# Kernel optimization log

Hardware: AMD Instinct MI355X
Metric: run time of the kernel (lower is better)

The kernel has to match this reference:

```python
import jax, jax.numpy as jnp
import numpy as np


def setup_inputs() -> dict:
    key = jax.random.key(0)
    ks = jax.random.split(key, 9)
    D, DK, DV = 512, 64, 64
    B, S = 4, 4096
    sd = 1.0 / np.sqrt(D).astype(np.float32)
    so = 1.0 / np.sqrt(DV).astype(np.float32)
    return {
        "x": jax.random.normal(ks[0], (B, S, D), dtype=jnp.float32),
        "Wq": jax.random.normal(ks[1], (D, DK), dtype=jnp.float32) * sd,
        "bq": jnp.zeros((DK,), dtype=jnp.float32),
        "Wk": jax.random.normal(ks[2], (D, DK), dtype=jnp.float32) * sd,
        "bk": jnp.zeros((DK,), dtype=jnp.float32),
        "Wv": jax.random.normal(ks[3], (D, DV), dtype=jnp.float32) * sd,
        "bv": jnp.zeros((DV,), dtype=jnp.float32),
        "Wo": jax.random.normal(ks[4], (DV, D), dtype=jnp.float32) * so,
        "bo": jnp.zeros((D,), dtype=jnp.float32),
    }


def reference(x, Wq, bq, Wk, bk, Wv, bv, Wo, bo):
    # x: (B, S, D)
    B, S, D = x.shape
    dk = Wq.shape[1]
    q = x @ Wq + bq            # (B, S, dk)
    k = x @ Wk + bk            # (B, S, dk)
    v = x @ Wv + bv            # (B, S, dv)
    scores = jnp.einsum("bik,bjk->bij", q, k) / jnp.sqrt(jnp.float32(dk))  # (B,S,S)
    # causal mask: True where j <= i (keep)
    causal = jnp.tril(jnp.ones((S, S), dtype=bool))
    scores = jnp.where(causal[None, :, :], scores, -jnp.inf)
    weights = jax.nn.softmax(scores, axis=-1)   # every row has >=1 unmasked entry
    out = jnp.einsum("bij,bjv->biv", weights, v)  # (B, S, dv)
    return out @ Wo + bo
```

## Files before the change

kernel.cpp:

```cpp
#include <hip/hip_runtime.h>
#include <hip/hip_bf16.h>

#define S_LEN 4096
#define D_MODEL 512
#define DKV 64
#define B_N 4
#define STR 72
#define VSTR 136

typedef __hip_bfloat16 bf16;
typedef __attribute__((ext_vector_type(8))) short short8;
typedef __attribute__((ext_vector_type(4))) float floatx4;

#define MFMA(a, b, c) __builtin_amdgcn_mfma_f32_16x16x32_bf16(a, b, c, 0, 0, 0)

__device__ __forceinline__ float b2f(bf16 v) { return __bfloat162float(v); }

__device__ __forceinline__ unsigned short f2bits(float v) {
    union { bf16 h; unsigned short u; } cv;
    cv.h = __float2bfloat16(v);
    return cv.u;
}
__device__ __forceinline__ float bits2f(unsigned short u) {
    union { bf16 h; unsigned short u; } cv;
    cv.u = u;
    return b2f(cv.h);
}

__global__ __launch_bounds__(64) void detect_kernel(const void* x, int* flag) {
    const int lane = threadIdx.x;
    const bf16* xb = (const bf16*)x;
    int bad = 0;
    for (int k = lane; k < 4096; k += 64) {
        float v = fabsf(b2f(xb[2 * k]));
        if (!(v < 64.f)) bad++;
    }
    #pragma unroll
    for (int off = 32; off >= 1; off >>= 1) bad += __shfl_xor(bad, off);
    if (lane == 0) *flag = (bad > 100) ? 1 : 0;
}

__global__ __launch_bounds__(512) void wprep_qkv_frag(
    const void* __restrict__ Wq, const void* __restrict__ bq,
    const void* __restrict__ Wk, const void* __restrict__ bk,
    const void* __restrict__ Wv, const void* __restrict__ bv,
    bf16* __restrict__ Wfh, bf16* __restrict__ Wfl, float* __restrict__ ball,
    const int* __restrict__ flag)
{
    __shared__ float xs[16][513];
    const int ct = blockIdx.x;
    const int c0 = ct * 16;
    const int g = c0 >> 6;
    const int cc0 = c0 & 63;
    const void* W    = (g == 0) ? Wq : (g == 1) ? Wk : Wv;
    const void* bias = (g == 0) ? bq : (g == 1) ? bk : bv;
    const int tid = threadIdx.x;
    const int f32 = *flag;

    #pragma unroll
    for (int i = 0; i < 16; ++i) {
        const int idx = tid + 512 * i;
        const int d = idx >> 4, j = idx & 15;
        const float v = f32 ? ((const float*)W)[(size_t)d * DKV + cc0 + j]
                            : b2f(((const bf16*)W)[(size_t)d * DKV + cc0 + j]);
        xs[j][d] = v;
    }
    __syncthreads();

    union Pack8 { uint4 u; unsigned short s[8]; };
    #pragma unroll
    for (int rep = 0; rep < 2; ++rep) {
        const int f = tid + rep * 512;
        const int kt = f >> 6, lane = f & 63;
        const int quad = lane >> 4, l15 = lane & 15;
        Pack8 ph, pl;
        #pragma unroll
        for (int j = 0; j < 8; ++j) {
            const float v = xs[l15][kt * 32 + quad * 8 + j];
            const unsigned short hb = f2bits(v);
            ph.s[j] = hb;
            pl.s[j] = f2bits(v - bits2f(hb));
        }
        const size_t o = (((size_t)ct * 16 + kt) * 64 + lane) * 8;
        *(uint4*)&Wfh[o] = ph.u;
        *(uint4*)&Wfl[o] = pl.u;
    }
    if (tid < 16)
        ball[c0 + tid] = f32 ? ((const float*)bias)[cc0 + tid]
                             : b2f(((const bf16*)bias)[cc0 + tid]);
}

__global__ __launch_bounds__(512) void wprep_o_frag(
    const void* __restrict__ Wo, const void* __restrict__ bo,
    bf16* __restrict__ WoFh, bf16* __restrict__ WoFl,
    float* __restrict__ ball2, const int* __restrict__ flag)
{
    __shared__ float ys[16][65];
    const int ctile = blockIdx.x;
    const int c0 = ctile * 16;
    const int tid = threadIdx.x;
    const int f32 = *flag;

    #pragma unroll
    for (int rep = 0; rep < 2; ++rep) {
        const int idx = tid + rep * 512;
        const int d = idx >> 4, j = idx & 15;
        const float v = f32 ? ((const float*)Wo)[(size_t)d * D_MODEL + c0 + j]
                            : b2f(((const bf16*)Wo)[(size_t)d * D_MODEL + c0 + j]);
        ys[j][d] = v;
    }
    __syncthreads();

    union Pack8 { uint4 u; unsigned short s[8]; };
    if (tid < 128) {
        const int kc = tid >> 6, lane = tid & 63;
        const int quad = lane >> 4, l15 = lane & 15;
        Pack8 ph, pl;
        #pragma unroll
        for (int j = 0; j < 8; ++j) {
            const float v = ys[l15][kc * 32 + quad * 8 + j];
            const unsigned short hb = f2bits(v);
            ph.s[j] = hb;
            pl.s[j] = f2bits(v - bits2f(hb));
        }
        const size_t o = (((size_t)ctile * 2 + kc) * 64 + lane) * 8;
        *(uint4*)&WoFh[o] = ph.u;
        *(uint4*)&WoFl[o] = pl.u;
    }
    if (tid < 16)
        ball2[c0 + tid] = f32 ? ((const float*)bo)[c0 + tid]
                              : b2f(((const bf16*)bo)[c0 + tid]);
}

__global__ __launch_bounds__(256) void qkv_mfma_bf16(
    const void* __restrict__ x,
    const bf16* __restrict__ Wfh, const float* __restrict__ ball,
    bf16* __restrict__ Qb, bf16* __restrict__ Kb, bf16* __restrict__ Vt,
    const int* __restrict__ flag)
{
    if (*flag) return;
    __shared__ unsigned short hiA[32 * D_MODEL];
    const int tid = threadIdx.x;
    const int rowBase = blockIdx.x * 32;

    const unsigned short* xr = (const unsigned short*)x + (size_t)rowBase * D_MODEL;
    #pragma unroll
    for (int i = 0; i < 8; ++i) {
        const int idx = tid + 256 * i;
        const int r = idx >> 6;
        const int c0 = (idx & 63) << 3;
        const uint4 hv = *(const uint4*)&xr[r * D_MODEL + c0];
        const int boff = (c0 * 2) ^ ((r & 7) << 4);
        *(uint4*)((char*)hiA + r * 1024 + boff) = hv;
    }
    __syncthreads();

    const int lane = tid & 63;
    const int w    = tid >> 6;
    const int quad = lane >> 4;
    const int l15  = lane & 15;
    const int wr   = w & 1;
    const int wcol = w >> 1;
    const int arow = wr * 16 + l15;
    const char* hib = (const char*)hiA + arow * 1024;
    const int swz = (arow & 7) << 4;

    floatx4 acc[6];
    #pragma unroll
    for (int ct = 0; ct < 6; ++ct) acc[ct] = (floatx4){0.f, 0.f, 0.f, 0.f};

    for (int kt = 0; kt < 16; ++kt) {
        const int boff = (kt * 64 + quad * 16) ^ swz;
        const short8 ah = *(const short8*)(hib + boff);
        #pragma unroll
        for (int ct = 0; ct < 6; ++ct) {
            const size_t fo = (((size_t)(wcol * 6 + ct) * 16 + kt) * 64 + lane) * 8;
            const short8 bh = *(const short8*)&Wfh[fo];
            acc[ct] = MFMA(ah, bh, acc[ct]);
        }
    }

    #pragma unroll
    for (int ct = 0; ct < 6; ++ct) {
        const int gc = wcol * 96 + ct * 16 + l15;
        const float bias = ball[gc];
        const float scale = (gc < 64) ? 0.18033688f : 1.0f;
        #pragma unroll
        for (int r = 0; r < 4; ++r) {
            const int gr = rowBase + wr * 16 + quad * 4 + r;
            const bf16 o = __float2bfloat16((acc[ct][r] + bias) * scale);
            if (gc < 64)       Qb[(size_t)gr * DKV + gc] = o;
            else if (gc < 128) Kb[(size_t)gr * DKV + (gc - 64)] = o;
            else {
                const int bb = gr >> 12, sidx = gr & (S_LEN - 1);
                Vt[((size_t)bb * DKV + (gc - 128)) * S_LEN + sidx] = o;
            }
        }
    }
}

__global__ __launch_bounds__(512) void qkv_mfma_f32(
    const void* __restrict__ x,
    const bf16* __restrict__ Wfh, const bf16* __restrict__ Wfl,
    const float* __restrict__ ball,
    bf16* __restrict__ Qb, bf16* __restrict__ Kb, bf16* __restrict__ Vt,
    const int* __restrict__ flag)
{
    if (!*flag) return;
    __shared__ unsigned short hiA[32 * D_MODEL];
    __shared__ unsigned short loA[32 * D_MODEL];
    const int tid = threadIdx.x;
    const int rowBase = blockIdx.x * 32;

    union Pack8 { uint4 u; unsigned short s[8]; };
    {
        const float* xr = (const float*)x + (size_t)rowBase * D_MODEL;
        #pragma unroll
        for (int i = 0; i < 4; ++i) {
            const int idx = tid + 512 * i;
            const int r = idx >> 6;
            const int c0 = (idx & 63) << 3;
            const float4 v0 = *(const float4*)&xr[r * D_MODEL + c0];
            const float4 v1 = *(const float4*)&xr[r * D_MODEL + c0 + 4];
            const float vv[8] = {v0.x, v0.y, v0.z, v0.w, v1.x, v1.y, v1.z, v1.w};
            Pack8 ph, pl;
            #pragma unroll
            for (int j = 0; j < 8; ++j) {
                const unsigned short hb = f2bits(vv[j]);
                ph.s[j] = hb;
                pl.s[j] = f2bits(vv[j] - bits2f(hb));
            }
            const int boff = (c0 * 2) ^ ((r & 7) << 4);
            *(uint4*)((char*)hiA + r * 1024 + boff) = ph.u;
            *(uint4*)((char*)loA + r * 1024 + boff) = pl.u;
        }
    }
    __syncthreads();

    const int lane = tid & 63;
    const int w    = tid >> 6;
    const int quad = lane >> 4;
    const int l15  = lane & 15;
    const int wr   = w & 1;
    const int wq   = w >> 1;
    const int arow = wr * 16 + l15;
    const char* hib = (const char*)hiA + arow * 1024;
    const char* lob = (const char*)loA + arow * 1024;
    const int swz = (arow & 7) << 4;

    floatx4 acc[3];
    #pragma unroll
    for (int ct = 0; ct < 3; ++ct) acc[ct] = (floatx4){0.f, 0.f, 0.f, 0.f};

    for (int kt = 0; kt < 16; ++kt) {
        const int boff = (kt * 64 + quad * 16) ^ swz;
        const short8 ah = *(const short8*)(hib + boff);
        const short8 al = *(const short8*)(lob + boff);
        #pragma unroll
        for (int ct = 0; ct < 3; ++ct) {
            const size_t fo = (((size_t)(wq * 3 + ct) * 16 + kt) * 64 + lane) * 8;
            const short8 bh = *(const short8*)&Wfh[fo];
            const short8 bl = *(const short8*)&Wfl[fo];
            acc[ct] = MFMA(ah, bh, acc[ct]);
            acc[ct] = MFMA(ah, bl, acc[ct]);
            acc[ct] = MFMA(al, bh, acc[ct]);
        }
    }

    #pragma unroll
    for (int ct = 0; ct < 3; ++ct) {
        const int gc = wq * 48 + ct * 16 + l15;
        const float bias = ball[gc];
        const float scale = (gc < 64) ? 0.18033688f : 1.0f;
        #pragma unroll
        for (int r = 0; r < 4; ++r) {
            const int gr = rowBase + wr * 16 + quad * 4 + r;
            const bf16 o = __float2bfloat16((acc[ct][r] + bias) * scale);
            if (gc < 64)       Qb[(size_t)gr * DKV + gc] = o;
            else if (gc < 128) Kb[(size_t)gr * DKV + (gc - 64)] = o;
            else {
                const int bb = gr >> 12, sidx = gr & (S_LEN - 1);
                Vt[((size_t)bb * DKV + (gc - 128)) * S_LEN + sidx] = o;
            }
        }
    }
}

__global__ __launch_bounds__(256, 3) void attn_mfma(
    const bf16* __restrict__ Qg, const bf16* __restrict__ Kg,
    const bf16* __restrict__ Vtg, float* __restrict__ Op,
    float* __restrict__ Mp, float* __restrict__ Lp)
{
    const int bid = blockIdx.x;
    const int xcd = bid & 7;
    const int b  = xcd >> 1;
    const int kh = xcd & 1;
    const int t  = 127 - (bid >> 3);
    const int rowBase = t * 32;
    const int tid = threadIdx.x;
    const int lane = tid & 63;
    const int w  = tid >> 6;
    const int wr = w & 1;
    const int wc = w >> 1;
    const int quad = lane >> 4;
    const int l15  = lane & 15;

    __shared__ bf16 Kl[128 * STR];
    __shared__ bf16 Vl[64 * VSTR];
    __shared__ bf16 Pl[32 * VSTR];
    __shared__ float redm[2][32];
    __shared__ float reds[2][32];

    const bf16* Qb = Qg + ((size_t)b * S_LEN + rowBase) * DKV;
    const bf16* Kb = Kg + (size_t)b * S_LEN * DKV;
    const bf16* Vb = Vtg + (size_t)b * DKV * S_LEN;

    {
        const int r = tid >> 3, d0q = (tid & 7) * 8;
        *(uint4*)&Pl[r * VSTR + d0q] = *(const uint4*)&Qb[r * DKV + d0q];
    }
    __syncthreads();
    short8 qf0, qf1;
    {
        const int qoff = (wr * 16 + l15) * VSTR + quad * 8;
        qf0 = *(const short8*)&Pl[qoff];
        qf1 = *(const short8*)&Pl[qoff + 32];
    }

    floatx4 acc0 = {0.f, 0.f, 0.f, 0.f}, acc1 = {0.f, 0.f, 0.f, 0.f};
    float m_run[4], l_run[4];
    #pragma unroll
    for (int r = 0; r < 4; ++r) { m_run[r] = -1e30f; l_run[r] = 0.f; }

    const int kbMax = (rowBase + 31) >> 7;
    const int kk = tid >> 1, dk = (tid & 1) * 32;
    const int vd = tid >> 2, vk = (tid & 3) * 32;

    uint4 kr0, kr1, kr2, kr3, vr0, vr1, vr2, vr3;
    int kb = kh;
    if (kb <= kbMax) {
        const uint4* ks = (const uint4*)&Kb[((size_t)(kb * 128 + kk)) * DKV + dk];
        kr0 = ks[0]; kr1 = ks[1]; kr2 = ks[2]; kr3 = ks[3];
        const uint4* vs = (const uint4*)&Vb[(size_t)vd * S_LEN + kb * 128 + vk];
        vr0 = vs[0]; vr1 = vs[1]; vr2 = vs[2]; vr3 = vs[3];
    }

    for (; kb <= kbMax; kb += 2) {
        __syncthreads();
        {
            uint4* kd = (uint4*)&Kl[kk * STR + dk];
            kd[0] = kr0; kd[1] = kr1; kd[2] = kr2; kd[3] = kr3;
            uint4* vdst = (uint4*)&Vl[vd * VSTR + vk];
            vdst[0] = vr0; vdst[1] = vr1; vdst[2] = vr2; vdst[3] = vr3;
        }
        __syncthreads();
        if (kb + 2 <= kbMax) {
            const uint4* ks = (const uint4*)&Kb[((size_t)((kb + 2) * 128 + kk)) * DKV + dk];
            kr0 = ks[0]; kr1 = ks[1]; kr2 = ks[2]; kr3 = ks[3];
            const uint4* vs = (const uint4*)&Vb[(size_t)vd * S_LEN + (kb + 2) * 128 + vk];
            vr0 = vs[0]; vr1 = vs[1]; vr2 = vs[2]; vr3 = vs[3];
        }

        floatx4 s[4];
        #pragma unroll
        for (int j = 0; j < 4; ++j) s[j] = (floatx4){0.f, 0.f, 0.f, 0.f};
        {
            const int qk = quad * 8;
            #pragma unroll
            for (int j = 0; j < 4; ++j) {
                const int kc = (wc * 64 + j * 16 + l15) * STR + qk;
                const short8 ba = *(const short8*)&Kl[kc];
                const short8 bb = *(const short8*)&Kl[kc + 32];
                s[j] = MFMA(qf0, ba, s[j]);
                s[j] = MFMA(qf1, bb, s[j]);
            }
        }
        if (kb == kbMax) {
            const int rowg = rowBase + wr * 16 + quad * 4;
            #pragma unroll
            for (int j = 0; j < 4; ++j) {
                const int kg = kb * 128 + wc * 64 + j * 16 + l15;
                #pragma unroll
                for (int r = 0; r < 4; ++r)
                    if (kg > rowg + r) s[j][r] = -1e30f;
            }
        }
        float m4[4];
        #pragma unroll
        for (int r = 0; r < 4; ++r)
            m4[r] = fmaxf(fmaxf(s[0][r], s[1][r]), fmaxf(s[2][r], s[3][r]));
        #pragma unroll
        for (int off = 1; off < 16; off <<= 1) {
            #pragma unroll
            for (int r = 0; r < 4; ++r) m4[r] = fmaxf(m4[r], __shfl_xor(m4[r], off));
        }
        if (l15 == 0) {
            #pragma unroll
            for (int r = 0; r < 4; ++r) redm[wc][wr * 16 + quad * 4 + r] = m4[r];
        }
        __syncthreads();
        float alpha[4], mnew[4];
        #pragma unroll
        for (int r = 0; r < 4; ++r) {
            const int row = wr * 16 + quad * 4 + r;
            const float mm = fmaxf(redm[0][row], redm[1][row]);
            mnew[r] = fmaxf(m_run[r], mm);
            alpha[r] = exp2f(m_run[r] - mnew[r]);
            m_run[r] = mnew[r];
        }
        float ps[4];
        #pragma unroll
        for (int r = 0; r < 4; ++r) {
            float acc_ps = 0.f;
            #pragma unroll
            for (int j = 0; j < 4; ++j) {
                const float p = exp2f(s[j][r] - mnew[r]);
                s[j][r] = p;
                acc_ps += p;
            }
            ps[r] = acc_ps;
        }
        #pragma unroll
        for (int off = 1; off < 16; off <<= 1) {
            #pragma unroll
            for (int r = 0; r < 4; ++r) ps[r] += __shfl_xor(ps[r], off);
        }
        if (l15 == 0) {
            #pragma unroll
            for (int r = 0; r < 4; ++r) reds[wc][wr * 16 + quad * 4 + r] = ps[r];
        }
        #pragma unroll
        for (int r = 0; r < 4; ++r) {
            acc0[r] *= alpha[r]; acc1[r] *= alpha[r];
            const int poff = (wr * 16 + quad * 4 + r) * VSTR + wc * 64 + l15;
            Pl[poff]      = __float2bfloat16(s[0][r]);
            Pl[poff + 16] = __float2bfloat16(s[1][r]);
            Pl[poff + 32] = __float2bfloat16(s[2][r]);
            Pl[poff + 48] = __float2bfloat16(s[3][r]);
        }
        __syncthreads();
        #pragma unroll
        for (int r = 0; r < 4; ++r) {
            const int row = wr * 16 + quad * 4 + r;
            l_run[r] = l_run[r] * alpha[r] + reds[0][row] + reds[1][row];
        }
        {
            const int pk = quad * 8;
            const int prow = (wr * 16 + l15) * VSTR;
            const int vrow0 = (wc * 32 + l15) * VSTR;
            const int vrow1 = vrow0 + 16 * VSTR;
            #pragma unroll
            for (int j = 0; j < 4; ++j) {
                const short8 pa  = *(const short8*)&Pl[prow + pk + j * 32];
                const short8 vb0 = *(const short8*)&Vl[vrow0 + pk + j * 32];
                const short8 vb1 = *(const short8*)&Vl[vrow1 + pk + j * 32];
                acc0 = MFMA(pa, vb0, acc0);
                acc1 = MFMA(pa, vb1, acc1);
            }
        }
    }
    #pragma unroll
    for (int r = 0; r < 4; ++r) {
        const int row = rowBase + wr * 16 + quad * 4 + r;
        float* op = Op + (((size_t)kh * B_N + b) * S_LEN + row) * DKV + wc * 32 + l15;
        op[0]  = acc0[r];
        op[16] = acc1[r];
    }
    if (wc == 0 && l15 == 0) {
        #pragma unroll
        for (int r = 0; r < 4; ++r) {
            const int row = rowBase + wr * 16 + quad * 4 + r;
            const size_t mi = (size_t)kh * B_N * S_LEN + (size_t)b * S_LEN + row;
            Mp[mi] = m_run[r];
            Lp[mi] = l_run[r];
        }
    }
}

__global__ __launch_bounds__(256) void merge_kernel(
    const float* __restrict__ Op, const float* __restrict__ Mp,
    const float* __restrict__ Lp, bf16* __restrict__ Oh, bf16* __restrict__ Ol)
{
    const int row = blockIdx.x * 32 + (threadIdx.x >> 3);
    const int d0 = (threadIdx.x & 7) * 8;
    const size_t half = (size_t)B_N * S_LEN;

    const float m0 = Mp[row], m1 = Mp[half + row];
    const float l0 = Lp[row], l1 = Lp[half + row];
    const float m = fmaxf(m0, m1);
    const float w0 = exp2f(m0 - m), w1 = exp2f(m1 - m);
    const float inv = 1.0f / (l0 * w0 + l1 * w1);

    const float* p0 = Op + (size_t)row * DKV + d0;
    const float* p1 = Op + half * DKV + (size_t)row * DKV + d0;
    union Pack8 { uint4 u; unsigned short s[8]; };
    Pack8 ph, pl;
    #pragma unroll
    for (int j = 0; j < 8; ++j) {
        const float o = (p0[j] * w0 + p1[j] * w1) * inv;
        const unsigned short hb = f2bits(o);
        ph.s[j] = hb;
        pl.s[j] = f2bits(o - bits2f(hb));
    }
    *(uint4*)&Oh[(size_t)row * DKV + d0] = ph.u;
    *(uint4*)&Ol[(size_t)row * DKV + d0] = pl.u;
}

#define PSTR 72
__global__ __launch_bounds__(256) void proj_mfma_bf16(
    const bf16* __restrict__ Oh, const bf16* __restrict__ Ol,
    const bf16* __restrict__ WoFh, const float* __restrict__ ball2,
    bf16* __restrict__ out, const int* __restrict__ flag)
{
    if (*flag) return;
    __shared__ unsigned short Ah[32 * PSTR], Al[32 * PSTR];
    const int tid = threadIdx.x;
    const int rowBase = blockIdx.x * 32;

    {
        const int r = tid >> 3, c0 = (tid & 7) * 8;
        *(uint4*)&Ah[r * PSTR + c0] = *(const uint4*)&Oh[(size_t)(rowBase + r) * DKV + c0];
        *(uint4*)&Al[r * PSTR + c0] = *(const uint4*)&Ol[(size_t)(rowBase + r) * DKV + c0];
    }
    __syncthreads();

    const int lane = tid & 63;
    const int w    = tid >> 6;
    const int quad = lane >> 4;
    const int l15  = lane & 15;
    const int wr   = w & 1;
    const int wcq  = w >> 1;

    const int aoff = (wr * 16 + l15) * PSTR + quad * 8;
    const short8 ah0 = *(const short8*)&Ah[aoff];
    const short8 ah1 = *(const short8*)&Ah[aoff + 32];
    const short8 al0 = *(const short8*)&Al[aoff];
    const short8 al1 = *(const short8*)&Al[aoff + 32];

    floatx4 acc[16];
    #pragma unroll
    for (int ct = 0; ct < 16; ++ct) acc[ct] = (floatx4){0.f, 0.f, 0.f, 0.f};

    #pragma unroll
    for (int ct = 0; ct < 16; ++ct) {
        const int ctile = wcq * 16 + ct;
        const size_t o0 = (((size_t)ctile * 2 + 0) * 64 + lane) * 8;
        const size_t o1 = (((size_t)ctile * 2 + 1) * 64 + lane) * 8;
        const short8 bh0 = *(const short8*)&WoFh[o0];
        const short8 bh1 = *(const short8*)&WoFh[o1];
        acc[ct] = MFMA(ah0, bh0, acc[ct]);
        acc[ct] = MFMA(ah1, bh1, acc[ct]);
        acc[ct] = MFMA(al0, bh0, acc[ct]);
        acc[ct] = MFMA(al1, bh1, acc[ct]);
    }

    #pragma unroll
    for (int ct = 0; ct < 16; ++ct) {
        const int col = wcq * 256 + ct * 16 + l15;
        const float bias = ball2[col];
        #pragma unroll
        for (int r = 0; r < 4; ++r) {
            const int row = rowBase + wr * 16 + quad * 4 + r;
            out[(size_t)row * D_MODEL + col] = __float2bfloat16(acc[ct][r] + bias);
        }
    }
}

__global__ __launch_bounds__(512) void proj_mfma_f32(
    const bf16* __restrict__ Oh, const bf16* __restrict__ Ol,
    const bf16* __restrict__ WoFh, const bf16* __restrict__ WoFl,
    const float* __restrict__ ball2, float* __restrict__ out,
    const int* __restrict__ flag)
{
    if (!*flag) return;
    __shared__ unsigned short Ah[32 * PSTR], Al[32 * PSTR];
    const int tid = threadIdx.x;
    const int rowBase = blockIdx.x * 32;

    {
        const int r = (tid & 255) >> 3, c0 = (tid & 7) * 8;
        if (tid < 256)
            *(uint4*)&Ah[r * PSTR + c0] = *(const uint4*)&Oh[(size_t)(rowBase + r) * DKV + c0];
        else
            *(uint4*)&Al[r * PSTR + c0] = *(const uint4*)&Ol[(size_t)(rowBase + r) * DKV + c0];
    }
    __syncthreads();

    const int lane = tid & 63;
    const int w    = tid >> 6;
    const int quad = lane >> 4;
    const int l15  = lane & 15;
    const int wr   = w & 1;
    const int wcq  = w >> 1;

    const int aoff = (wr * 16 + l15) * PSTR + quad * 8;
    const short8 ah0 = *(const short8*)&Ah[aoff];
    const short8 ah1 = *(const short8*)&Ah[aoff + 32];
    const short8 al0 = *(const short8*)&Al[aoff];
    const short8 al1 = *(const short8*)&Al[aoff + 32];

    floatx4 acc[8];
    #pragma unroll
    for (int ct = 0; ct < 8; ++ct) acc[ct] = (floatx4){0.f, 0.f, 0.f, 0.f};

    #pragma unroll
    for (int ct = 0; ct < 8; ++ct) {
        const int ctile = wcq * 8 + ct;
        const size_t o0 = (((size_t)ctile * 2 + 0) * 64 + lane) * 8;
        const size_t o1 = (((size_t)ctile * 2 + 1) * 64 + lane) * 8;
        const short8 bh0 = *(const short8*)&WoFh[o0];
        const short8 bh1 = *(const short8*)&WoFh[o1];
        const short8 bl0 = *(const short8*)&WoFl[o0];
        const short8 bl1 = *(const short8*)&WoFl[o1];
        acc[ct] = MFMA(ah0, bh0, acc[ct]);
        acc[ct] = MFMA(ah1, bh1, acc[ct]);
        acc[ct] = MFMA(ah0, bl0, acc[ct]);
        acc[ct] = MFMA(ah1, bl1, acc[ct]);
        acc[ct] = MFMA(al0, bh0, acc[ct]);
        acc[ct] = MFMA(al1, bh1, acc[ct]);
    }

    #pragma unroll
    for (int ct = 0; ct < 8; ++ct) {
        const int col = wcq * 128 + ct * 16 + l15;
        const float bias = ball2[col];
        #pragma unroll
        for (int r = 0; r < 4; ++r) {
            const int row = rowBase + wr * 16 + quad * 4 + r;
            out[(size_t)row * D_MODEL + col] = acc[ct][r] + bias;
        }
    }
}

extern "C" void kernel_launch(void* const* d_in, const int* in_sizes, int n_in,
                              void* d_out, int out_size, void* d_ws, size_t ws_size,
                              hipStream_t stream) {
    const void* x  = d_in[0];
    const void* Wq = d_in[1];
    const void* bq = d_in[2];
    const void* Wk = d_in[3];
    const void* bk = d_in[4];
    const void* Wv = d_in[5];
    const void* bv = d_in[6];
    const void* Wo = d_in[7];
    const void* bo = d_in[8];

    const int rows = B_N * S_LEN;
    char* p = (char*)d_ws;
    int*  flag = (int*)p;                          p += 256;
    bf16* Qb = (bf16*)p;                           p += (size_t)rows * DKV * 2;
    bf16* Kb = (bf16*)p;                           p += (size_t)rows * DKV * 2;
    bf16* Vt = (bf16*)p;                           p += (size_t)rows * DKV * 2;
    bf16* Wfh = (bf16*)p;                          p += (size_t)12 * 16 * 64 * 8 * 2;
    bf16* Wfl = (bf16*)p;                          p += (size_t)12 * 16 * 64 * 8 * 2;
    float* ball = (float*)p;                       p += 1024;
    bf16* WoFh = (bf16*)p;                         p += (size_t)32 * 2 * 64 * 8 * 2;
    bf16* WoFl = (bf16*)p;                         p += (size_t)32 * 2 * 64 * 8 * 2;
    float* ball2 = (float*)p;                      p += D_MODEL * 4;
    float* Op = (float*)p;                         p += (size_t)2 * rows * DKV * 4;
    float* Mp = (float*)p;                         p += (size_t)2 * rows * 4;
    float* Lp = (float*)p;                         p += (size_t)2 * rows * 4;
    bf16* Ohb = (bf16*)p;                          p += (size_t)rows * DKV * 2;
    bf16* Olb = (bf16*)p;                          p += (size_t)rows * DKV * 2;

    detect_kernel<<<1, 64, 0, stream>>>(x, flag);
    wprep_qkv_frag<<<12, 512, 0, stream>>>(Wq, bq, Wk, bk, Wv, bv, Wfh, Wfl, ball, flag);
    wprep_o_frag<<<32, 512, 0, stream>>>(Wo, bo, WoFh, WoFl, ball2, flag);
    qkv_mfma_bf16<<<512, 256, 0, stream>>>(x, Wfh, ball, Qb, Kb, Vt, flag);
    qkv_mfma_f32<<<512, 512, 0, stream>>>(x, Wfh, Wfl, ball, Qb, Kb, Vt, flag);
    attn_mfma<<<1024, 256, 0, stream>>>(Qb, Kb, Vt, Op, Mp, Lp);
    merge_kernel<<<512, 256, 0, stream>>>(Op, Mp, Lp, Ohb, Olb);
    proj_mfma_bf16<<<512, 256, 0, stream>>>(Ohb, Olb, WoFh, ball2, (bf16*)d_out, flag);
    proj_mfma_f32<<<512, 512, 0, stream>>>(Ohb, Olb, WoFh, WoFl, ball2, (float*)d_out, flag);
}
```

Measured before the change: 189.9 us.

## Use 64-row query tiles with per-wave full key rows and configurable KV splits

The attention kernel now gives each block 64 query rows, and each wave owns 16 rows across all 128 keys. This removes the cross-wave max/sum reductions through shared memory and two block barriers per key tile, and makes each K/V tile load serve twice as many queries. The number of key splits becomes 4 when the workspace is large enough (2 otherwise), keeping the grid size, and the merge kernel is generalised to NS partials. The cost is more registers per thread (8 score tiles, 4 accumulators), more partial output traffic through merge, and a shared-memory P buffer that is now synchronised only with a waitcnt instead of a barrier.

```diff
diff --git a/kernel.cpp b/kernel.cpp
--- a/kernel.cpp
+++ b/kernel.cpp
@@ -289,50 +289,51 @@
 __global__ __launch_bounds__(256, 3) void attn_mfma(
     const bf16* __restrict__ Qg, const bf16* __restrict__ Kg,
     const bf16* __restrict__ Vtg, float* __restrict__ Op,
-    float* __restrict__ Mp, float* __restrict__ Lp)
+    float* __restrict__ Mp, float* __restrict__ Lp, const int NS)
 {
     const int bid = blockIdx.x;
     const int xcd = bid & 7;
-    const int b  = xcd >> 1;
-    const int kh = xcd & 1;
-    const int t  = 127 - (bid >> 3);
-    const int rowBase = t * 32;
+    const int rest = bid >> 3;
+    const int b   = xcd >> 1;
+    const int khH = (NS == 4) ? (rest & 1) : 0;
+    const int t64 = 63 - ((NS == 4) ? (rest >> 1) : rest);
+    const int kh  = khH * 2 + (xcd & 1);
+    const int rowBase = t64 * 64;
     const int tid = threadIdx.x;
     const int lane = tid & 63;
     const int w  = tid >> 6;
-    const int wr = w & 1;
-    const int wc = w >> 1;
     const int quad = lane >> 4;
     const int l15  = lane & 15;
 
     __shared__ bf16 Kl[128 * STR];
     __shared__ bf16 Vl[64 * VSTR];
-    __shared__ bf16 Pl[32 * VSTR];
-    __shared__ float redm[2][32];
-    __shared__ float reds[2][32];
+    __shared__ bf16 Pl[64 * VSTR];
 
     const bf16* Qb = Qg + ((size_t)b * S_LEN + rowBase) * DKV;
     const bf16* Kb = Kg + (size_t)b * S_LEN * DKV;
     const bf16* Vb = Vtg + (size_t)b * DKV * S_LEN;
 
     {
-        const int r = tid >> 3, d0q = (tid & 7) * 8;
-        *(uint4*)&Pl[r * VSTR + d0q] = *(const uint4*)&Qb[r * DKV + d0q];
+        const int qr = tid >> 2, qd = (tid & 3) * 16;
+        *(uint4*)&Pl[qr * VSTR + qd]     = *(const uint4*)&Qb[qr * DKV + qd];
+        *(uint4*)&Pl[qr * VSTR + qd + 8] = *(const uint4*)&Qb[qr * DKV + qd + 8];
     }
     __syncthreads();
     short8 qf0, qf1;
     {
-        const int qoff = (wr * 16 + l15) * VSTR + quad * 8;
+        const int qoff = (w * 16 + l15) * VSTR + quad * 8;
         qf0 = *(const short8*)&Pl[qoff];
         qf1 = *(const short8*)&Pl[qoff + 32];
     }
 
-    floatx4 acc0 = {0.f, 0.f, 0.f, 0.f}, acc1 = {0.f, 0.f, 0.f, 0.f};
+    floatx4 acc[4];
+    #pragma unroll
+    for (int v = 0; v < 4; ++v) acc[v] = (floatx4){0.f, 0.f, 0.f, 0.f};
     float m_run[4], l_run[4];
     #pragma unroll
     for (int r = 0; r < 4; ++r) { m_run[r] = -1e30f; l_run[r] = 0.f; }
 
-    const int kbMax = (rowBase + 31) >> 7;
+    const int kbMax = (rowBase + 63) >> 7;
     const int kk = tid >> 1, dk = (tid & 1) * 32;
     const int vd = tid >> 2, vk = (tid & 3) * 32;
 
@@ -345,7 +346,7 @@
         vr0 = vs[0]; vr1 = vs[1]; vr2 = vs[2]; vr3 = vs[3];
     }
 
-    for (; kb <= kbMax; kb += 2) {
+    for (; kb <= kbMax; kb += NS) {
         __syncthreads();
         {
             uint4* kd = (uint4*)&Kl[kk * STR + dk];
@@ -354,69 +355,66 @@
             vdst[0] = vr0; vdst[1] = vr1; vdst[2] = vr2; vdst[3] = vr3;
         }
         __syncthreads();
-        if (kb + 2 <= kbMax) {
-            const uint4* ks = (const uint4*)&Kb[((size_t)((kb + 2) * 128 + kk)) * DKV + dk];
+        if (kb + NS <= kbMax) {
+            const uint4* ks = (const uint4*)&Kb[((size_t)((kb + NS) * 128 + kk)) * DKV + dk];
             kr0 = ks[0]; kr1 = ks[1]; kr2 = ks[2]; kr3 = ks[3];
-            const uint4* vs = (const uint4*)&Vb[(size_t)vd * S_LEN + (kb + 2) * 128 + vk];
+            const uint4* vs = (const uint4*)&Vb[(size_t)vd * S_LEN + (kb + NS) * 128 + vk];
             vr0 = vs[0]; vr1 = vs[1]; vr2 = vs[2]; vr3 = vs[3];
         }
 
-        floatx4 s[4];
-        #pragma unroll
-        for (int j = 0; j < 4; ++j) s[j] = (floatx4){0.f, 0.f, 0.f, 0.f};
+        floatx4 s[8];
+        #pragma unroll
+        for (int jt = 0; jt < 8; ++jt) s[jt] = (floatx4){0.f, 0.f, 0.f, 0.f};
         {
             const int qk = quad * 8;
             #pragma unroll
-            for (int j = 0; j < 4; ++j) {
-                const int kc = (wc * 64 + j * 16 + l15) * STR + qk;
+            for (int jt = 0; jt < 8; ++jt) {
+                const int kc = (jt * 16 + l15) * STR + qk;
                 const short8 ba = *(const short8*)&Kl[kc];
                 const short8 bb = *(const short8*)&Kl[kc + 32];
-                s[j] = MFMA(qf0, ba, s[j]);
-                s[j] = MFMA(qf1, bb, s[j]);
+                s[jt] = MFMA(qf0, ba, s[jt]);
+                s[jt] = MFMA(qf1, bb, s[jt]);
             }
         }
         if (kb == kbMax) {
-            const int rowg = rowBase + wr * 16 + quad * 4;
-            #pragma unroll
-            for (int j = 0; j < 4; ++j) {
-                const int kg = kb * 128 + wc * 64 + j * 16 + l15;
+            const int rowg = rowBase + w * 16 + quad * 4;
+            #pragma unroll
+            for (int jt = 0; jt < 8; ++jt) {
+                const int kg = kb * 128 + jt * 16 + l15;
                 #pragma unroll
                 for (int r = 0; r < 4; ++r)
-                    if (kg > rowg + r) s[j][r] = -1e30f;
+                    if (kg > rowg + r) s[jt][r] = -1e30f;
             }
         }
         float m4[4];
         #pragma unroll
-        for (int r = 0; r < 4; ++r)
-            m4[r] = fmaxf(fmaxf(s[0][r], s[1][r]), fmaxf(s[2][r], s[3][r]));
+        for (int r = 0; r < 4; ++r) {
+            float mm = s[0][r];
+            #pragma unroll
+            for (int jt = 1; jt < 8; ++jt) mm = fmaxf(mm, s[jt][r]);
+            m4[r] = mm;
+        }
         #pragma unroll
         for (int off = 1; off < 16; off <<= 1) {
             #pragma unroll
             for (int r = 0; r < 4; ++r) m4[r] = fmaxf(m4[r], __shfl_xor(m4[r], off));
         }
-        if (l15 == 0) {
-            #pragma unroll
-            for (int r = 0; r < 4; ++r) redm[wc][wr * 16 + quad * 4 + r] = m4[r];
-        }
-        __syncthreads();
-        float alpha[4], mnew[4];
-        #pragma unroll
-        for (int r = 0; r < 4; ++r) {
-            const int row = wr * 16 + quad * 4 + r;
-            const float mm = fmaxf(redm[0][row], redm[1][row]);
-            mnew[r] = fmaxf(m_run[r], mm);
-            alpha[r] = exp2f(m_run[r] - mnew[r]);
-            m_run[r] = mnew[r];
+        float alpha[4];
+        #pragma unroll
+        for (int r = 0; r < 4; ++r) {
+            const float mnew = fmaxf(m_run[r], m4[r]);
+            alpha[r] = exp2f(m_run[r] - mnew);
+            m_run[r] = mnew;
         }
         float ps[4];
         #pragma unroll
         for (int r = 0; r < 4; ++r) {
             float acc_ps = 0.f;
             #pragma unroll
-            for (int j = 0; j < 4; ++j) {
-                const float p = exp2f(s[j][r] - mnew[r]);
-                s[j][r] = p;
-                acc_ps += p;
+            for (int jt = 0; jt < 8; ++jt) {
+                const float pp = exp2f(s[jt][r] - m_run[r]);
+                s[jt][r] = pp;
+                acc_ps += pp;
             }
             ps[r] = acc_ps;
         }
@@ -425,52 +423,48 @@
             #pragma unroll
             for (int r = 0; r < 4; ++r) ps[r] += __shfl_xor(ps[r], off);
         }
-        if (l15 == 0) {
-            #pragma unroll
-            for (int r = 0; r < 4; ++r) reds[wc][wr * 16 + quad * 4 + r] = ps[r];
-        }
-        #pragma unroll
-        for (int r = 0; r < 4; ++r) {
-            acc0[r] *= alpha[r]; acc1[r] *= alpha[r];
-            const int poff = (wr * 16 + quad * 4 + r) * VSTR + wc * 64 + l15;
-            Pl[poff]      = __float2bfloat16(s[0][r]);
-            Pl[poff + 16] = __float2bfloat16(s[1][r]);
-            Pl[poff + 32] = __float2bfloat16(s[2][r]);
-            Pl[poff + 48] = __float2bfloat16(s[3][r]);
-        }
-        __syncthreads();
-        #pragma unroll
-        for (int r = 0; r < 4; ++r) {
-            const int row = wr * 16 + quad * 4 + r;
-            l_run[r] = l_run[r] * alpha[r] + reds[0][row] + reds[1][row];
-        }
+        #pragma unroll
+        for (int r = 0; r < 4; ++r) {
+            l_run[r] = l_run[r] * alpha[r] + ps[r];
+            #pragma unroll
+            for (int v = 0; v < 4; ++v) acc[v][r] *= alpha[r];
+            const int poff = (w * 16 + quad * 4 + r) * VSTR + l15;
+            #pragma unroll
+            for (int jt = 0; jt < 8; ++jt)
+                Pl[poff + jt * 16] = __float2bfloat16(s[jt][r]);
+        }
+        asm volatile("s_waitcnt lgkmcnt(0)" ::: "memory");
+
         {
             const int pk = quad * 8;
-            const int prow = (wr * 16 + l15) * VSTR;
-            const int vrow0 = (wc * 32 + l15) * VSTR;
-            const int vrow1 = vrow0 + 16 * VSTR;
-            #pragma unroll
-            for (int j = 0; j < 4; ++j) {
-                const short8 pa  = *(const short8*)&Pl[prow + pk + j * 32];
-                const short8 vb0 = *(const short8*)&Vl[vrow0 + pk + j * 32];
-                const short8 vb1 = *(const short8*)&Vl[vrow1 + pk + j * 32];
-                acc0 = MFMA(pa, vb0, acc0);
-                acc1 = MFMA(pa, vb1, acc1);
+            const int prow = (w * 16 + l15) * VSTR;
+            short8 pa[4];
+            #pragma unroll
+            for (int c = 0; c < 4; ++c)
+                pa[c] = *(const short8*)&Pl[prow + pk + c * 32];
+            #pragma unroll
+            for (int v = 0; v < 4; ++v) {
+                const int vrow = (v * 16 + l15) * VSTR;
+                #pragma unroll
+                for (int c = 0; c < 4; ++c) {
+                    const short8 vb = *(const short8*)&Vl[vrow + pk + c * 32];
+                    acc[v] = MFMA(pa[c], vb, acc[v]);
+                }
             }
         }
     }
     #pragma unroll
     for (int r = 0; r < 4; ++r) {
-        const int row = rowBase + wr * 16 + quad * 4 + r;
-        float* op = Op + (((size_t)kh * B_N + b) * S_LEN + row) * DKV + wc * 32 + l15;
-        op[0]  = acc0[r];
-        op[16] = acc1[r];
-    }
-    if (wc == 0 && l15 == 0) {
-        #pragma unroll
-        for (int r = 0; r < 4; ++r) {
-            const int row = rowBase + wr * 16 + quad * 4 + r;
-            const size_t mi = (size_t)kh * B_N * S_LEN + (size_t)b * S_LEN + row;
+        const int row = rowBase + w * 16 + quad * 4 + r;
+        float* op = Op + (((size_t)kh * B_N + b) * S_LEN + row) * DKV + l15;
+        #pragma unroll
+        for (int v = 0; v < 4; ++v) op[v * 16] = acc[v][r];
+    }
+    if (l15 == 0) {
+        #pragma unroll
+        for (int r = 0; r < 4; ++r) {
+            const int row = rowBase + w * 16 + quad * 4 + r;
+            const size_t mi = ((size_t)kh * B_N + b) * S_LEN + row;
             Mp[mi] = m_run[r];
             Lp[mi] = l_run[r];
         }
@@ -479,28 +473,39 @@
 
 __global__ __launch_bounds__(256) void merge_kernel(
     const float* __restrict__ Op, const float* __restrict__ Mp,
-    const float* __restrict__ Lp, bf16* __restrict__ Oh, bf16* __restrict__ Ol)
+    const float* __restrict__ Lp, bf16* __restrict__ Oh, bf16* __restrict__ Ol,
+    const int NS)
 {
     const int row = blockIdx.x * 32 + (threadIdx.x >> 3);
     const int d0 = (threadIdx.x & 7) * 8;
-    const size_t half = (size_t)B_N * S_LEN;
-
-    const float m0 = Mp[row], m1 = Mp[half + row];
-    const float l0 = Lp[row], l1 = Lp[half + row];
-    const float m = fmaxf(m0, m1);
-    const float w0 = exp2f(m0 - m), w1 = exp2f(m1 - m);
-    const float inv = 1.0f / (l0 * w0 + l1 * w1);
-
-    const float* p0 = Op + (size_t)row * DKV + d0;
-    const float* p1 = Op + half * DKV + (size_t)row * DKV + d0;
+    const size_t part = (size_t)B_N * S_LEN;
+
+    float m = -1e30f;
+    #pragma unroll 4
+    for (int i = 0; i < NS; ++i) m = fmaxf(m, Mp[i * part + row]);
+
+    float oacc[8];
+    #pragma unroll
+    for (int jj = 0; jj < 8; ++jj) oacc[jj] = 0.f;
+    float denom = 0.f;
+    #pragma unroll 4
+    for (int i = 0; i < NS; ++i) {
+        const float wi = exp2f(Mp[i * part + row] - m);
+        denom += Lp[i * part + row] * wi;
+        const float* pi = Op + (i * part + row) * DKV + d0;
+        #pragma unroll
+        for (int jj = 0; jj < 8; ++jj) oacc[jj] += pi[jj] * wi;
+    }
+    const float inv = 1.0f / denom;
+
     union Pack8 { uint4 u; unsigned short s[8]; };
     Pack8 ph, pl;
     #pragma unroll
-    for (int j = 0; j < 8; ++j) {
-        const float o = (p0[j] * w0 + p1[j] * w1) * inv;
+    for (int jj = 0; jj < 8; ++jj) {
+        const float o = oacc[jj] * inv;
         const unsigned short hb = f2bits(o);
-        ph.s[j] = hb;
-        pl.s[j] = f2bits(o - bits2f(hb));
+        ph.s[jj] = hb;
+        pl.s[jj] = f2bits(o - bits2f(hb));
     }
     *(uint4*)&Oh[(size_t)row * DKV + d0] = ph.u;
     *(uint4*)&Ol[(size_t)row * DKV + d0] = pl.u;
@@ -646,6 +651,8 @@
     const void* bo = d_in[8];
 
     const int rows = B_N * S_LEN;
+    const int NS = (ws_size >= (size_t)30 * 1024 * 1024) ? 4 : 2;
+
     char* p = (char*)d_ws;
     int*  flag = (int*)p;                          p += 256;
     bf16* Qb = (bf16*)p;                           p += (size_t)rows * DKV * 2;
@@ -657,9 +664,9 @@
     bf16* WoFh = (bf16*)p;                         p += (size_t)32 * 2 * 64 * 8 * 2;
     bf16* WoFl = (bf16*)p;                         p += (size_t)32 * 2 * 64 * 8 * 2;
     float* ball2 = (float*)p;                      p += D_MODEL * 4;
-    float* Op = (float*)p;                         p += (size_t)2 * rows * DKV * 4;
-    float* Mp = (float*)p;                         p += (size_t)2 * rows * 4;
-    float* Lp = (float*)p;                         p += (size_t)2 * rows * 4;
+    float* Op = (float*)p;                         p += (size_t)NS * rows * DKV * 4;
+    float* Mp = (float*)p;                         p += (size_t)NS * rows * 4;
+    float* Lp = (float*)p;                         p += (size_t)NS * rows * 4;
     bf16* Ohb = (bf16*)p;                          p += (size_t)rows * DKV * 2;
     bf16* Olb = (bf16*)p;                          p += (size_t)rows * DKV * 2;
 
@@ -668,8 +675,8 @@
     wprep_o_frag<<<32, 512, 0, stream>>>(Wo, bo, WoFh, WoFl, ball2, flag);
     qkv_mfma_bf16<<<512, 256, 0, stream>>>(x, Wfh, ball, Qb, Kb, Vt, flag);
     qkv_mfma_f32<<<512, 512, 0, stream>>>(x, Wfh, Wfl, ball, Qb, Kb, Vt, flag);
-    attn_mfma<<<1024, 256, 0, stream>>>(Qb, Kb, Vt, Op, Mp, Lp);
-    merge_kernel<<<512, 256, 0, stream>>>(Op, Mp, Lp, Ohb, Olb);
+    attn_mfma<<<256 * NS, 256, 0, stream>>>(Qb, Kb, Vt, Op, Mp, Lp, NS);
+    merge_kernel<<<512, 256, 0, stream>>>(Op, Mp, Lp, Ohb, Olb, NS);
     proj_mfma_bf16<<<512, 256, 0, stream>>>(Ohb, Olb, WoFh, ball2, (bf16*)d_out, flag);
     proj_mfma_f32<<<512, 512, 0, stream>>>(Ohb, Olb, WoFh, WoFl, ball2, (float*)d_out, flag);
 }
```

New measurement: 181.9 us. -4.2%, faster.
